# Kernel optimization log

Hardware: AMD Instinct MI355X
Metric: run time of the kernel (lower is better)

## Reference

```python
import jax, jax.numpy as jnp
import numpy as np
from jax import lax

B, L = 4, 2500
Y = 8922
VOCAB = 50002  # vocab_size + 2
E = 100        # embed_size
F = 50         # num_filter_maps
K = 9          # kernel_size
PAD = K // 2


def setup_inputs() -> dict:
    key = jax.random.key(0)
    ks = jax.random.split(key, 8)
    x = jax.random.randint(ks[0], (B, L), 0, VOCAB)
    target = jax.random.uniform(ks[1], (B, Y), dtype=jnp.float32)
    embed_table = jax.random.normal(ks[2], (VOCAB, E), dtype=jnp.float32) * 0.1
    embed_table = embed_table.at[0].set(0.0)  # padding_idx=0
    conv_w = jax.random.normal(ks[3], (F, E, K), dtype=jnp.float32) * (1.0 / np.sqrt(E * K))
    conv_b = jax.random.normal(ks[4], (F,), dtype=jnp.float32) * 0.01
    U_w = jax.random.normal(ks[5], (Y, F), dtype=jnp.float32) * (1.0 / np.sqrt(F))
    final_w = jax.random.normal(ks[6], (Y, F), dtype=jnp.float32) * (1.0 / np.sqrt(F))
    final_b = jax.random.normal(ks[7], (Y,), dtype=jnp.float32) * 0.01
    return {"x": x, "target": target, "embed_table": embed_table,
            "conv_w": conv_w, "conv_b": conv_b, "U_w": U_w,
            "final_w": final_w, "final_b": final_b}


def reference(x, target, embed_table, conv_w, conv_b, U_w, final_w, final_b):
    # embedding lookup (padding_idx=0 rows are zero); dropout is eval-mode identity
    e = embed_table[x] * (x != 0)[..., None].astype(embed_table.dtype)  # [B, L, E]
    # conv1d over sequence: input NCH [B, E, L], kernel OIH [F, E, K], 'same' padding
    h = lax.conv_general_dilated(e.transpose(0, 2, 1), conv_w, (1,), [(PAD, PAD)],
                                 dimension_numbers=("NCH", "OIH", "NCH"))
    h = jnp.tanh(h + conv_b[None, :, None]).transpose(0, 2, 1)  # [B, L, F]
    # label-wise attention
    scores = jnp.einsum("yf,blf->byl", U_w, h)      # [B, Y, L]
    alpha = jax.nn.softmax(scores, axis=2)            # [B, Y, L]
    m = jnp.einsum("byl,blf->byf", alpha, h)         # [B, Y, F]
    y = jnp.einsum("yf,byf->by", final_w, m) + final_b  # [B, Y]
    # BCE with logits, mean reduction
    loss = jnp.mean(jnp.maximum(y, 0.0) - y * target + jnp.log1p(jnp.exp(-jnp.abs(y))))
    yhat = jax.nn.sigmoid(y)
    return (yhat, loss, alpha)
```

## Files before the change

kernel.cpp:

```cpp
#include <hip/hip_runtime.h>
#include <hip/hip_bf16.h>
#include <math.h>

#define B_ 4
#define L_ 2500
#define Y_ 8922
#define E_ 100
#define F_ 50
#define K_ 9

typedef __attribute__((ext_vector_type(8))) short bfrag8;
typedef __attribute__((ext_vector_type(4))) float ffrag4;

#define WS_CWT_F  0
#define WS_HB_U16 90000
#define WS_M_F    295000
#define WS_PART_F 2079400
#define NBLK_FINAL 140

__global__ __launch_bounds__(256) void k0_cwt(const float* __restrict__ conv_w,
                                              float* __restrict__ cwT) {
    int idx = blockIdx.x * 256 + threadIdx.x;
    if (idx < F_ * E_ * K_) {
        int f = idx / (E_ * K_);
        int r = idx % (E_ * K_);
        int e = r / K_;
        int k = r % K_;
        cwT[f * (E_ * K_) + k * E_ + e] = conv_w[idx];
    }
}

#define LT1 32
__global__ __launch_bounds__(256) void k1_embed_conv(
    const int* __restrict__ x, const float* __restrict__ emb_tab,
    const float* __restrict__ cwT, const float* __restrict__ conv_b,
    unsigned short* __restrict__ hb) {
    __shared__ __align__(16) float smem[(LT1 + 8) * E_];
    int b = blockIdx.y;
    int l0 = blockIdx.x * LT1;
    int tid = threadIdx.x;
    for (int idx = tid; idx < (LT1 + 8) * E_; idx += 256) {
        int r = idx / E_, e = idx % E_;
        int l = l0 + r - 4;
        float v = 0.f;
        if (l >= 0 && l < L_) {
            int tok = x[b * L_ + l];
            if (tok != 0) v = emb_tab[tok * E_ + e];
        }
        smem[idx] = v;
    }
    __syncthreads();
    const float4* s4 = (const float4*)smem;
    const float4* w4 = (const float4*)cwT;
    for (int idx = tid; idx < LT1 * F_; idx += 256) {
        int ll = idx / F_, f = idx % F_;
        int l = l0 + ll;
        if (l >= L_) continue;
        float acc = conv_b[f];
        for (int k = 0; k < K_; ++k) {
            const float4* se = s4 + (ll + k) * (E_ / 4);
            const float4* we = w4 + f * (E_ * K_ / 4) + k * (E_ / 4);
#pragma unroll
            for (int e4 = 0; e4 < E_ / 4; ++e4) {
                float4 a = se[e4];
                float4 w = we[e4];
                acc += a.x * w.x + a.y * w.y + a.z * w.z + a.w * w.w;
            }
        }
        __hip_bfloat16 hv = __float2bfloat16(tanhf(acc));
        hb[(size_t)(b * L_ + l) * F_ + f] = *reinterpret_cast<unsigned short*>(&hv);
    }
}

#define YT 64
#define LT 64
#define NLT ((L_ + LT - 1) / LT)
#define HSTR 72
__global__ __launch_bounds__(256) void k2_attn(
    const float* __restrict__ Uw, const unsigned short* __restrict__ hb,
    float* __restrict__ m, float* __restrict__ alpha) {
    __shared__ unsigned short hlf[64][HSTR];
    __shared__ unsigned short hfl[64][HSTR];
    __shared__ unsigned short psh[4][16][HSTR];

    int b = blockIdx.y;
    int y0 = blockIdx.x * YT;
    int tid = threadIdx.x;
    int wv = tid >> 6;
    int lane = tid & 63;
    int col = lane & 15;
    int quad = lane >> 4;
    int ywb = y0 + wv * 16;
    int ym = ywb + col;

    bfrag8 uf[2];
#pragma unroll
    for (int kc = 0; kc < 2; ++kc) {
#pragma unroll
        for (int j = 0; j < 8; ++j) {
            int f = kc * 32 + quad * 8 + j;
            float v = (ym < Y_ && f < F_) ? Uw[(size_t)ym * F_ + f] : 0.f;
            __hip_bfloat16 bv = __float2bfloat16(v);
            uf[kc][j] = *reinterpret_cast<short*>(&bv);
        }
    }

    for (int i = tid; i < 64 * 14; i += 256) {
        int r = i / 14, c = 50 + (i % 14);
        hlf[r][c] = 0;
    }
    for (int i = tid; i < 14 * 64; i += 256) {
        int r = 50 + i / 64, c = i % 64;
        hfl[r][c] = (r == 50) ? (unsigned short)0x3F80 : (unsigned short)0;
    }

    ffrag4 macc[4];
#pragma unroll
    for (int nt = 0; nt < 4; ++nt) macc[nt] = (ffrag4){0.f, 0.f, 0.f, 0.f};

    const unsigned short* hbase = hb + (size_t)b * L_ * F_;

    for (int lt = 0; lt < NLT; ++lt) {
        int l0 = lt * LT;
        __syncthreads();
        const unsigned int* src = (const unsigned int*)(hbase + (size_t)l0 * F_);
        for (int d = tid; d < LT * F_ / 2; d += 256) {
            int r = d / 25, c = d % 25;
            unsigned int v = (l0 + r < L_) ? src[d] : 0u;
            *(unsigned int*)&hlf[r][2 * c] = v;
            hfl[2 * c][r] = (unsigned short)(v & 0xFFFF);
            hfl[2 * c + 1][r] = (unsigned short)(v >> 16);
        }
        __syncthreads();
#pragma unroll
        for (int nt = 0; nt < 4; ++nt) {
            ffrag4 s = (ffrag4){0.f, 0.f, 0.f, 0.f};
#pragma unroll
            for (int kc = 0; kc < 2; ++kc) {
                bfrag8 bf = *(const bfrag8*)&hlf[nt * 16 + col][kc * 32 + quad * 8];
                s = __builtin_amdgcn_mfma_f32_16x16x32_bf16(uf[kc], bf, s, 0, 0, 0);
            }
            int l = l0 + nt * 16 + col;
#pragma unroll
            for (int i = 0; i < 4; ++i) {
                float e = (l < L_) ? __expf(s[i]) : 0.f;
                __hip_bfloat16 be = __float2bfloat16(e);
                psh[wv][quad * 4 + i][nt * 16 + col] = *reinterpret_cast<unsigned short*>(&be);
            }
        }
        __syncthreads();
#pragma unroll
        for (int kc = 0; kc < 2; ++kc) {
            bfrag8 af = *(const bfrag8*)&psh[wv][col][kc * 32 + quad * 8];
#pragma unroll
            for (int nt = 0; nt < 4; ++nt) {
                bfrag8 bf = *(const bfrag8*)&hfl[nt * 16 + col][kc * 32 + quad * 8];
                macc[nt] = __builtin_amdgcn_mfma_f32_16x16x32_bf16(af, bf, macc[nt], 0, 0, 0);
            }
        }
    }

    float rd[4];
#pragma unroll
    for (int i = 0; i < 4; ++i) {
        float d = __shfl(macc[3][i], quad * 16 + 2, 64);
        rd[i] = 1.0f / d;
    }
#pragma unroll
    for (int nt = 0; nt < 4; ++nt) {
        int f = nt * 16 + col;
        if (f < F_) {
#pragma unroll
            for (int i = 0; i < 4; ++i) {
                int y = ywb + quad * 4 + i;
                if (y < Y_) m[((size_t)b * Y_ + y) * F_ + f] = macc[nt][i] * rd[i];
            }
        }
    }

    float* aout = alpha + (size_t)b * Y_ * L_;
    for (int lt = 0; lt < NLT; ++lt) {
        int l0 = lt * LT;
        __syncthreads();
        const unsigned int* src = (const unsigned int*)(hbase + (size_t)l0 * F_);
        for (int d = tid; d < LT * F_ / 2; d += 256) {
            int r = d / 25, c = d % 25;
            unsigned int v = (l0 + r < L_) ? src[d] : 0u;
            *(unsigned int*)&hlf[r][2 * c] = v;
        }
        __syncthreads();
#pragma unroll
        for (int nt = 0; nt < 4; ++nt) {
            ffrag4 s = (ffrag4){0.f, 0.f, 0.f, 0.f};
#pragma unroll
            for (int kc = 0; kc < 2; ++kc) {
                bfrag8 bf = *(const bfrag8*)&hlf[nt * 16 + col][kc * 32 + quad * 8];
                s = __builtin_amdgcn_mfma_f32_16x16x32_bf16(uf[kc], bf, s, 0, 0, 0);
            }
            int l = l0 + nt * 16 + col;
            if (l < L_) {
#pragma unroll
                for (int i = 0; i < 4; ++i) {
                    int y = ywb + quad * 4 + i;
                    if (y < Y_) aout[(size_t)y * L_ + l] = __expf(s[i]) * rd[i];
                }
            }
        }
    }
}

__global__ __launch_bounds__(256) void k4_final(
    const float* __restrict__ m, const float* __restrict__ fw,
    const float* __restrict__ fb, const float* __restrict__ target,
    float* __restrict__ yhat, float* __restrict__ part) {
    int idx = blockIdx.x * 256 + threadIdx.x;
    float term = 0.f;
    if (idx < B_ * Y_) {
        int yy = idx % Y_;
        const float* mr = m + (size_t)idx * F_;
        const float* wr = fw + (size_t)yy * F_;
        float s = fb[yy];
#pragma unroll
        for (int f = 0; f < F_; ++f) s += mr[f] * wr[f];
        yhat[idx] = 1.f / (1.f + __expf(-s));
        float t = target[idx];
        term = fmaxf(s, 0.f) - s * t + log1pf(__expf(-fabsf(s)));
    }
    float v = term;
    for (int off = 32; off > 0; off >>= 1) v += __shfl_down(v, off, 64);
    __shared__ float red[4];
    int lane = threadIdx.x & 63, w = threadIdx.x >> 6;
    if (lane == 0) red[w] = v;
    __syncthreads();
    if (threadIdx.x == 0) part[blockIdx.x] = red[0] + red[1] + red[2] + red[3];
}

__global__ __launch_bounds__(256) void k5_loss(const float* __restrict__ part,
                                               float* __restrict__ loss_out) {
    float v = 0.f;
    for (int i = threadIdx.x; i < NBLK_FINAL; i += 256) v += part[i];
    for (int off = 32; off > 0; off >>= 1) v += __shfl_down(v, off, 64);
    __shared__ float red[4];
    int lane = threadIdx.x & 63, w = threadIdx.x >> 6;
    if (lane == 0) red[w] = v;
    __syncthreads();
    if (threadIdx.x == 0) loss_out[0] = (red[0] + red[1] + red[2] + red[3]) / (float)(B_ * Y_);
}

extern "C" void kernel_launch(void* const* d_in, const int* in_sizes, int n_in,
                              void* d_out, int out_size, void* d_ws, size_t ws_size,
                              hipStream_t stream) {
    const int*   x       = (const int*)d_in[0];
    const float* target  = (const float*)d_in[1];
    const float* emb_tab = (const float*)d_in[2];
    const float* conv_w  = (const float*)d_in[3];
    const float* conv_b  = (const float*)d_in[4];
    const float* U_w     = (const float*)d_in[5];
    const float* final_w = (const float*)d_in[6];
    const float* final_b = (const float*)d_in[7];

    float* out = (float*)d_out;
    float* wsf = (float*)d_ws;
    unsigned short* wsu = (unsigned short*)d_ws;

    float* cwT            = wsf + WS_CWT_F;
    unsigned short* hbf   = wsu + WS_HB_U16;
    float* mbuf           = wsf + WS_M_F;
    float* part           = wsf + WS_PART_F;

    float* yhat  = out;
    float* loss  = out + (size_t)B_ * Y_;
    float* alpha = loss + 1;

    k0_cwt<<<(F_ * E_ * K_ + 255) / 256, 256, 0, stream>>>(conv_w, cwT);
    k1_embed_conv<<<dim3((L_ + LT1 - 1) / LT1, B_), 256, 0, stream>>>(x, emb_tab, cwT, conv_b, hbf);
    k2_attn<<<dim3((Y_ + YT - 1) / YT, B_), 256, 0, stream>>>(U_w, hbf, mbuf, alpha);
    k4_final<<<NBLK_FINAL, 256, 0, stream>>>(mbuf, final_w, final_b, target, yhat, part);
    k5_loss<<<1, 256, 0, stream>>>(part, loss);
}
```

Measured before the change: 809.4 us.

## Split attention kernel into L-chunked denominator/context and alpha kernels

The single attention kernel, which ran two full passes over the sequence per label tile, becomes two kernels that each handle one chunk of the sequence per block. The first accumulates the unnormalized context vectors and softmax denominators into zeroed workspace with float atomics. The second recomputes scores and writes normalized alpha using those denominators, and normalization of m moves into the final kernel. This raises the block count far above the CU count to fix low occupancy, at the cost of atomics, two memsets and recomputing scores across kernels.

```diff
diff --git a/kernel.cpp b/kernel.cpp
--- a/kernel.cpp
+++ b/kernel.cpp
@@ -13,10 +13,15 @@
 typedef __attribute__((ext_vector_type(4))) float ffrag4;
 
 #define WS_CWT_F  0
+#define WS_DEN_F  0
 #define WS_HB_U16 90000
 #define WS_M_F    295000
 #define WS_PART_F 2079400
 #define NBLK_FINAL 140
+
+__device__ __forceinline__ void atomAddF(float* p, float v) {
+    unsafeAtomicAdd(p, v);
+}
 
 __global__ __launch_bounds__(256) void k0_cwt(const float* __restrict__ conv_w,
                                               float* __restrict__ cwT) {
@@ -75,16 +80,20 @@
 #define YT 64
 #define LT 64
 #define NLT ((L_ + LT - 1) / LT)
+#define NYB ((Y_ + YT - 1) / YT)
 #define HSTR 72
-__global__ __launch_bounds__(256) void k2_attn(
+#define CH1 4
+#define TPC1 (NLT / CH1)
+__global__ __launch_bounds__(256) void k2a_denm(
     const float* __restrict__ Uw, const unsigned short* __restrict__ hb,
-    float* __restrict__ m, float* __restrict__ alpha) {
+    float* __restrict__ mws, float* __restrict__ den) {
     __shared__ unsigned short hlf[64][HSTR];
     __shared__ unsigned short hfl[64][HSTR];
     __shared__ unsigned short psh[4][16][HSTR];
 
-    int b = blockIdx.y;
+    int b = blockIdx.z;
     int y0 = blockIdx.x * YT;
+    int ch = blockIdx.y;
     int tid = threadIdx.x;
     int wv = tid >> 6;
     int lane = tid & 63;
@@ -120,7 +129,7 @@
 
     const unsigned short* hbase = hb + (size_t)b * L_ * F_;
 
-    for (int lt = 0; lt < NLT; ++lt) {
+    for (int lt = ch * TPC1; lt < ch * TPC1 + TPC1; ++lt) {
         int l0 = lt * LT;
         __syncthreads();
         const unsigned int* src = (const unsigned int*)(hbase + (size_t)l0 * F_);
@@ -160,26 +169,69 @@
         }
     }
 
-    float rd[4];
-#pragma unroll
-    for (int i = 0; i < 4; ++i) {
-        float d = __shfl(macc[3][i], quad * 16 + 2, 64);
-        rd[i] = 1.0f / d;
-    }
 #pragma unroll
     for (int nt = 0; nt < 4; ++nt) {
         int f = nt * 16 + col;
-        if (f < F_) {
-#pragma unroll
-            for (int i = 0; i < 4; ++i) {
-                int y = ywb + quad * 4 + i;
-                if (y < Y_) m[((size_t)b * Y_ + y) * F_ + f] = macc[nt][i] * rd[i];
-            }
-        }
-    }
-
+#pragma unroll
+        for (int i = 0; i < 4; ++i) {
+            int y = ywb + quad * 4 + i;
+            if (y < Y_) {
+                if (f < F_) {
+                    atomAddF(&mws[((size_t)b * Y_ + y) * F_ + f], macc[nt][i]);
+                } else if (f == F_) {
+                    atomAddF(&den[(size_t)b * Y_ + y], macc[nt][i]);
+                }
+            }
+        }
+    }
+}
+
+#define CH2 10
+#define TPC2 (NLT / CH2)
+__global__ __launch_bounds__(256) void k2b_alpha(
+    const float* __restrict__ Uw, const unsigned short* __restrict__ hb,
+    const float* __restrict__ den, float* __restrict__ alpha) {
+    __shared__ unsigned short hlf[64][HSTR];
+
+    int b = blockIdx.z;
+    int y0 = blockIdx.x * YT;
+    int ch = blockIdx.y;
+    int tid = threadIdx.x;
+    int wv = tid >> 6;
+    int lane = tid & 63;
+    int col = lane & 15;
+    int quad = lane >> 4;
+    int ywb = y0 + wv * 16;
+    int ym = ywb + col;
+
+    bfrag8 uf[2];
+#pragma unroll
+    for (int kc = 0; kc < 2; ++kc) {
+#pragma unroll
+        for (int j = 0; j < 8; ++j) {
+            int f = kc * 32 + quad * 8 + j;
+            float v = (ym < Y_ && f < F_) ? Uw[(size_t)ym * F_ + f] : 0.f;
+            __hip_bfloat16 bv = __float2bfloat16(v);
+            uf[kc][j] = *reinterpret_cast<short*>(&bv);
+        }
+    }
+
+    float rd[4];
+#pragma unroll
+    for (int i = 0; i < 4; ++i) {
+        int y = ywb + quad * 4 + i;
+        rd[i] = (y < Y_) ? 1.0f / den[(size_t)b * Y_ + y] : 0.f;
+    }
+
+    for (int i = tid; i < 64 * 14; i += 256) {
+        int r = i / 14, c = 50 + (i % 14);
+        hlf[r][c] = 0;
+    }
+
+    const unsigned short* hbase = hb + (size_t)b * L_ * F_;
     float* aout = alpha + (size_t)b * Y_ * L_;
-    for (int lt = 0; lt < NLT; ++lt) {
+
+    for (int lt = ch * TPC2; lt < ch * TPC2 + TPC2; ++lt) {
         int l0 = lt * LT;
         __syncthreads();
         const unsigned int* src = (const unsigned int*)(hbase + (size_t)l0 * F_);
@@ -210,18 +262,20 @@
 }
 
 __global__ __launch_bounds__(256) void k4_final(
-    const float* __restrict__ m, const float* __restrict__ fw,
-    const float* __restrict__ fb, const float* __restrict__ target,
-    float* __restrict__ yhat, float* __restrict__ part) {
+    const float* __restrict__ m, const float* __restrict__ den,
+    const float* __restrict__ fw, const float* __restrict__ fb,
+    const float* __restrict__ target, float* __restrict__ yhat,
+    float* __restrict__ part) {
     int idx = blockIdx.x * 256 + threadIdx.x;
     float term = 0.f;
     if (idx < B_ * Y_) {
         int yy = idx % Y_;
         const float* mr = m + (size_t)idx * F_;
         const float* wr = fw + (size_t)yy * F_;
-        float s = fb[yy];
-#pragma unroll
-        for (int f = 0; f < F_; ++f) s += mr[f] * wr[f];
+        float dot = 0.f;
+#pragma unroll
+        for (int f = 0; f < F_; ++f) dot += mr[f] * wr[f];
+        float s = fb[yy] + dot / den[idx];
         yhat[idx] = 1.f / (1.f + __expf(-s));
         float t = target[idx];
         term = fmaxf(s, 0.f) - s * t + log1pf(__expf(-fabsf(s)));
@@ -264,6 +318,7 @@
     unsigned short* wsu = (unsigned short*)d_ws;
 
     float* cwT            = wsf + WS_CWT_F;
+    float* den            = wsf + WS_DEN_F;
     unsigned short* hbf   = wsu + WS_HB_U16;
     float* mbuf           = wsf + WS_M_F;
     float* part           = wsf + WS_PART_F;
@@ -274,7 +329,10 @@
 
     k0_cwt<<<(F_ * E_ * K_ + 255) / 256, 256, 0, stream>>>(conv_w, cwT);
     k1_embed_conv<<<dim3((L_ + LT1 - 1) / LT1, B_), 256, 0, stream>>>(x, emb_tab, cwT, conv_b, hbf);
-    k2_attn<<<dim3((Y_ + YT - 1) / YT, B_), 256, 0, stream>>>(U_w, hbf, mbuf, alpha);
-    k4_final<<<NBLK_FINAL, 256, 0, stream>>>(mbuf, final_w, final_b, target, yhat, part);
+    hipMemsetAsync(den, 0, (size_t)B_ * Y_ * sizeof(float), stream);
+    hipMemsetAsync(mbuf, 0, (size_t)B_ * Y_ * F_ * sizeof(float), stream);
+    k2a_denm<<<dim3(NYB, CH1, B_), 256, 0, stream>>>(U_w, hbf, mbuf, den);
+    k2b_alpha<<<dim3(NYB, CH2, B_), 256, 0, stream>>>(U_w, hbf, den, alpha);
+    k4_final<<<NBLK_FINAL, 256, 0, stream>>>(mbuf, den, final_w, final_b, target, yhat, part);
     k5_loss<<<1, 256, 0, stream>>>(part, loss);
 }
```

Measured after the change: 850.5 us. 5.1% more time.
